# Performance work log

Measured on AMD Instinct MI355X. Metric: run time of the kernel, lower is better.

Reference implementation:

```python
import jax, jax.numpy as jnp
import numpy as np

H = 20  # GRU hidden size (fixed in the module)


def gru_cell(x, h, Wih, Whh, bih, bhh):
    # PyTorch GRU cell math. x: (B, F), h: (B, H)
    gi = x @ Wih.T + bih  # (B, 3H)
    gh = h @ Whh.T + bhh  # (B, 3H)
    i_r, i_z, i_n = jnp.split(gi, 3, axis=-1)
    h_r, h_z, h_n = jnp.split(gh, 3, axis=-1)
    r = jax.nn.sigmoid(i_r + h_r)
    z = jax.nn.sigmoid(i_z + h_z)
    n = jnp.tanh(i_n + r * h_n)
    return (1.0 - z) * n + z * h


def setup_inputs() -> dict:
    key = jax.random.key(0)
    ks = jax.random.split(key, 16)
    B, S, R = 1024, 1024, 12
    F = R + 4 + 4 + 8 + 8  # 36 = input_record_width + embedding output_dim
    x = jax.random.normal(ks[0], (B, S, R), dtype=jnp.float32)
    onehots = jax.random.randint(ks[1], (B, S, 4), 0, 10, dtype=jnp.int64)
    s = 0.1
    inp = {
        'x': x, 'onehots': onehots,
        'emb0': jax.random.normal(ks[2], (10, 4), jnp.float32) * s,
        'emb1': jax.random.normal(ks[3], (20, 4), jnp.float32) * s,
        'emb2': jax.random.normal(ks[4], (50, 8), jnp.float32) * s,
        'emb3': jax.random.normal(ks[5], (100, 8), jnp.float32) * s,
        'Wih1': jax.random.normal(ks[6], (3 * H, F), jnp.float32) * s,
        'Whh1': jax.random.normal(ks[7], (3 * H, H), jnp.float32) * s,
        'bih1': jax.random.normal(ks[8], (3 * H,), jnp.float32) * s,
        'bhh1': jax.random.normal(ks[9], (3 * H,), jnp.float32) * s,
        'Wih2': jax.random.normal(ks[10], (3 * H, F), jnp.float32) * s,
        'Whh2': jax.random.normal(ks[11], (3 * H, H), jnp.float32) * s,
        'bih2': jax.random.normal(ks[12], (3 * H,), jnp.float32) * s,
        'bhh2': jax.random.normal(ks[13], (3 * H,), jnp.float32) * s,
        'Wfc': jax.random.normal(ks[14], (F, H), jnp.float32) * s,
        'bfc': jax.random.normal(ks[15], (F,), jnp.float32) * s,
    }
    return inp


def reference(x, onehots, emb0, emb1, emb2, emb3,
              Wih1, Whh1, bih1, bhh1, Wih2, Whh2, bih2, bhh2, Wfc, bfc):
    # Onehot embedding: lookup per categorical column, concat
    emb = jnp.concatenate([
        emb0[onehots[..., 0]], emb1[onehots[..., 1]],
        emb2[onehots[..., 2]], emb3[onehots[..., 3]],
    ], axis=-1)
    xin = jnp.concatenate([x, emb], axis=-1)  # (B, S, F)
    origin = xin
    B, S, F = xin.shape

    # Encoder GRU (gru1) over the sequence; keep only final hidden state
    h0 = jnp.zeros((B, H), xin.dtype)

    def enc_step(h, xt):
        return gru_cell(xt, h, Wih1, Whh1, bih1, bhh1), None

    h_last, _ = jax.lax.scan(enc_step, h0, jnp.swapaxes(xin, 0, 1))
    h = jnp.tanh(h_last)
    x0 = jnp.tanh(h @ Wfc.T + bfc)  # first decoded step

    def dec_step(carry, _):
        xprev, hprev = carry
        hnew = jnp.tanh(gru_cell(xprev, hprev, Wih2, Whh2, bih2, bhh2))
        xnew = jnp.tanh(hnew @ Wfc.T + bfc)
        return (xnew, hnew), xnew

    _, rest = jax.lax.scan(dec_step, (x0, h), None, length=S - 1)  # (S-1, B, F)
    xs = jnp.concatenate([x0[None], rest], axis=0)  # (S, B, F)
    xs = jnp.swapaxes(xs, 0, 1)[:, ::-1]  # (B, S, F), flipped along time
    return (origin, xs)
```

## Files before the change

### kernel.cpp

```cpp
#include <hip/hip_runtime.h>

#define BATCH 1024
#define SEQ   1024
#define FDIM  36
#define HID   20
#define G3    60
#define CR    64
#define NCHUNK (SEQ/CR)

typedef float v2f __attribute__((ext_vector_type(2)));

__device__ __forceinline__ float fast_sigmoid(float x){
    return __builtin_amdgcn_rcpf(1.0f + __expf(-x));
}
__device__ __forceinline__ float fast_tanh(float x){
    return fmaf(-2.0f, __builtin_amdgcn_rcpf(1.0f + __expf(2.0f*x)), 1.0f);
}

__global__ __launch_bounds__(128, 2)
void gru_fused(const float* __restrict__ x,
               const int* __restrict__ oh,
               const float* __restrict__ e0, const float* __restrict__ e1,
               const float* __restrict__ e2, const float* __restrict__ e3,
               const float* __restrict__ Wih1g, const float* __restrict__ Whh1g,
               const float* __restrict__ bih1g, const float* __restrict__ bhh1g,
               const float* __restrict__ Wih2g, const float* __restrict__ Whh2g,
               const float* __restrict__ bih2g, const float* __restrict__ bhh2g,
               const float* __restrict__ Wfcg,  const float* __restrict__ bfcg,
               float* __restrict__ origin, float* __restrict__ out2)
{
    __shared__ __align__(16) float gbuf[2][CR][G3];
    __shared__ __align__(16) float psh[64];
    __shared__ __align__(16) float dsh[64];
    __shared__ __align__(16) float hsh[64];

    const int lane   = threadIdx.x & 63;
    const bool is_enc = (threadIdx.x < 64);
    const int b = __builtin_amdgcn_readfirstlane(blockIdx.x);

    const int k = lane < G3 ? lane : G3 - 1;

    float whh1[HID];
    float bh1 = 0.f;
    float hs[HID];
    float hv = 0.0f;
    if (is_enc) {
        #pragma unroll
        for (int u = 0; u < HID; u++) whh1[u] = Whh1g[k * HID + u];
        bh1 = bhh1g[k];
        #pragma unroll
        for (int u = 0; u < HID; u++) hs[u] = 0.0f;
    }

    const int j = lane;
    const float* tbl; int ohc, eshift, sub;
    if (j < 16)      { tbl = e0; ohc = 0; eshift = 2; sub = j - 12; }
    else if (j < 20) { tbl = e1; ohc = 1; eshift = 2; sub = j - 16; }
    else if (j < 28) { tbl = e2; ohc = 2; eshift = 3; sub = j - 20; }
    else             { tbl = e3; ohc = 3; eshift = 3; sub = j - 28; }
    if (sub < 0) sub = 0;
    if (sub > 7) sub = 7;
    const bool from_x = (j < 12);
    const float* pa = from_x ? (x + j) : (tbl + sub);
    v2f w1p[FDIM/2]; float bi1 = 0.f;
    if (!is_enc) {
        #pragma unroll
        for (int q = 0; q < FDIM/2; q++) w1p[q] = ((const v2f*)(Wih1g + k * FDIM))[q];
        bi1 = bih1g[k];
    }

#define HS_BCAST(HVAL) do {                                                  \
        hsh[lane] = (HVAL);                                                  \
        const float4* hq_ = (const float4*)hsh;                              \
        float4 t0_ = hq_[0], t1_ = hq_[1], t2_ = hq_[2], t3_ = hq_[3],       \
               t4_ = hq_[4];                                                 \
        hs[0]=t0_.x;  hs[1]=t0_.y;  hs[2]=t0_.z;  hs[3]=t0_.w;               \
        hs[4]=t1_.x;  hs[5]=t1_.y;  hs[6]=t1_.z;  hs[7]=t1_.w;               \
        hs[8]=t2_.x;  hs[9]=t2_.y;  hs[10]=t2_.z; hs[11]=t2_.w;              \
        hs[12]=t3_.x; hs[13]=t3_.y; hs[14]=t3_.z; hs[15]=t3_.w;              \
        hs[16]=t4_.x; hs[17]=t4_.y; hs[18]=t4_.z; hs[19]=t4_.w;              \
    } while (0)

#define GATE_STEP(GIV, WHH, BH, HVAR) do {                                   \
        float h0 = BH, h1 = 0.f, h2 = 0.f, h3 = 0.f;                         \
        _Pragma("unroll")                                                    \
        for (int uu = 0; uu < HID; uu += 4) {                                \
            h0 = fmaf(WHH[uu + 0], hs[uu + 0], h0);                          \
            h1 = fmaf(WHH[uu + 1], hs[uu + 1], h1);                          \
            h2 = fmaf(WHH[uu + 2], hs[uu + 2], h2);                          \
            h3 = fmaf(WHH[uu + 3], hs[uu + 3], h3);                          \
        }                                                                    \
        float gh = (h0 + h1) + (h2 + h3);                                    \
        float v   = (GIV) + gh;                                              \
        float in_ = __shfl((GIV),(lane + 40) & 63);                          \
        float hn  = __shfl(gh,   (lane + 40) & 63);                          \
        float s = fast_sigmoid(v);                        \
        float z = __shfl(s, (lane + 20) & 63);  \
        float n = fast_tanh(fmaf(s, hn, in_));                               \
        HVAR = n + z * (HVAR - n);                                           \
        HS_BCAST(HVAR);                                                      \
    } while (0)

#define CONSUME_CHUNK(CB) do {                                               \
        const float* gp = &gbuf[CB][0][k];                                   \
        float ga = gp[0], gbv = gp[G3];                                      \
        _Pragma("unroll 1")                                                  \
        for (int i = 0; i < CR; i += 2) {                                    \
            float ge = ga, go = gbv;                                         \
            if (i < CR - 2) ga = gp[(i + 2) * G3];                           \
            GATE_STEP(ge, whh1, bh1, hv);                                    \
            if (i < CR - 2) gbv = gp[(i + 3) * G3];                          \
            GATE_STEP(go, whh1, bh1, hv);                                    \
        }                                                                    \
    } while (0)

    #pragma unroll 1
    for (int c = 0; c < NCHUNK; ++c) {
        if (!is_enc) {
            const int rbase = b * SEQ + c * CR;
            float* gdst = &gbuf[c & 1][0][0];
            const float4* xp4 = (const float4*)psh;
            #pragma unroll 1
            for (int g = 0; g < CR / 8; ++g) {
                int ohv[8];
                #pragma unroll
                for (int n = 0; n < 8; n++)
                    ohv[n] = oh[(rbase + 8 * g + n) * 4 + ohc];
                float valv[8];
                #pragma unroll
                for (int n = 0; n < 8; n++) {
                    int R = rbase + 8 * g + n;
                    int off = from_x ? (R * 12) : (ohv[n] << eshift);
                    valv[n] = pa[off];
                }
                #pragma unroll
                for (int n = 0; n < 8; n++) {
                    const int i = 8 * g + n;
                    const size_t R = (size_t)(rbase + i);
                    psh[lane] = valv[n];
                    if (lane < FDIM) origin[R * FDIM + lane] = valv[n];
                    v2f a0 = {bi1, 0.f}, a1 = {0.f, 0.f};
                    #pragma unroll
                    for (int q = 0; q < 9; q++) {
                        float4 xv4 = xp4[q];
                        v2f xlo = {xv4.x, xv4.y}, xhi = {xv4.z, xv4.w};
                        a0 = __builtin_elementwise_fma(w1p[2*q],     xlo, a0);
                        a1 = __builtin_elementwise_fma(w1p[2*q + 1], xhi, a1);
                    }
                    float gg = (a0.x + a1.x) + (a0.y + a1.y);
                    if (lane < G3) gdst[i * G3 + lane] = gg;
                }
            }
        } else if (c > 0) {
            CONSUME_CHUNK((c - 1) & 1);
        }
        __syncthreads();
    }
    if (!is_enc) return;

    CONSUME_CHUNK((NCHUNK - 1) & 1);

    const int kf = lane < FDIM ? lane : FDIM - 1;
    float whh2[HID], wfc[HID];
    v2f wih2p[FDIM/2];
    #pragma unroll
    for (int q = 0; q < FDIM/2; q++) wih2p[q] = ((const v2f*)(Wih2g + k * FDIM))[q];
    #pragma unroll
    for (int u = 0; u < HID; u++) whh2[u] = Whh2g[k * HID + u];
    #pragma unroll
    for (int u = 0; u < HID; u++) wfc[u] = Wfcg[kf * HID + u];
    const float bi2 = bih2g[k], bh2 = bhh2g[k];
    const float bf  = bfcg[kf];

    float hvd = fast_tanh(hv);
    HS_BCAST(hvd);

    float* orow = out2 + ((size_t)b * SEQ + (SEQ - 1)) * FDIM;
    const v2f* xp = (const v2f*)dsh;

    float xv0;
    {
        float f0 = bf, f1 = 0.f, f2 = 0.f, f3 = 0.f;
        #pragma unroll
        for (int u = 0; u < HID; u += 4) {
            f0 = fmaf(wfc[u + 0], hs[u + 0], f0);
            f1 = fmaf(wfc[u + 1], hs[u + 1], f1);
            f2 = fmaf(wfc[u + 2], hs[u + 2], f2);
            f3 = fmaf(wfc[u + 3], hs[u + 3], f3);
        }
        xv0 = fast_tanh((f0 + f1) + (f2 + f3));
    }
    dsh[lane] = xv0;
    v2f xsA[FDIM/2], xsB[FDIM/2];
    #pragma unroll
    for (int q = 0; q < FDIM/2; q++) xsA[q] = xp[q];
    if (lane < FDIM) orow[lane] = xv0;

#define DEC_STEP(XSIN, XSOUT, XST) do {                                      \
        float h0 = bh2, h1 = 0.f, h2 = 0.f, h3 = 0.f;                        \
        _Pragma("unroll")                                                    \
        for (int u = 0; u < HID; u += 4) {                                   \
            h0 = fmaf(whh2[u + 0], hs[u + 0], h0);                           \
            h1 = fmaf(whh2[u + 1], hs[u + 1], h1);                           \
            h2 = fmaf(whh2[u + 2], hs[u + 2], h2);                           \
            h3 = fmaf(whh2[u + 3], hs[u + 3], h3);                           \
        }                                                                    \
        float gh = (h0 + h1) + (h2 + h3);                                    \
        v2f accA = {bi2, 0.f}, accB = {0.f, 0.f};                            \
        _Pragma("unroll")                                                    \
        for (int q = 0; q < FDIM/2; q += 2) {                                \
            accA = __builtin_elementwise_fma(wih2p[q],     XSIN[q],     accA); \
            accB = __builtin_elementwise_fma(wih2p[q + 1], XSIN[q + 1], accB); \
        }                                                                    \
        float gi = (accA.x + accB.x) + (accA.y + accB.y);                    \
        float v   = gi + gh;                                                 \
        float in_ = __shfl(gi, (lane + 40) & 63);                            \
        float hn  = __shfl(gh, (lane + 40) & 63);                            \
        float s = fast_sigmoid(v);                                           \
        float z = __shfl(s, (lane + 20) & 63);                               \
        float n = fast_tanh(fmaf(s, hn, in_));                               \
        float hraw = n + z * (hvd - n);                                      \
        hvd = fast_tanh(hraw);                                               \
        HS_BCAST(hvd);                                                       \
        float f0 = bf, f1 = 0.f, f2 = 0.f, f3 = 0.f;                         \
        _Pragma("unroll")                                                    \
        for (int u = 0; u < HID; u += 4) {                                   \
            f0 = fmaf(wfc[u + 0], hs[u + 0], f0);                            \
            f1 = fmaf(wfc[u + 1], hs[u + 1], f1);                            \
            f2 = fmaf(wfc[u + 2], hs[u + 2], f2);                            \
            f3 = fmaf(wfc[u + 3], hs[u + 3], f3);                            \
        }                                                                    \
        XST = fast_tanh((f0 + f1) + (f2 + f3));                              \
        orow -= FDIM;                                                        \
        dsh[lane] = XST;                  \
        _Pragma("unroll")                                                    \
        for (int q = 0; q < FDIM/2; q++) XSOUT[q] = xp[q];    \
        if (lane < FDIM) orow[lane] = XST;                                   \
    } while (0)

    float xvA, xvB;
    #pragma unroll 1
    for (int i = 0; i < (SEQ - 2) / 2; ++i) {
        DEC_STEP(xsA, xsB, xvA);
        DEC_STEP(xsB, xsA, xvB);
    }
    DEC_STEP(xsA, xsB, xvA);
}

extern "C" void kernel_launch(void* const* d_in, const int* in_sizes, int n_in,
                              void* d_out, int out_size, void* d_ws, size_t ws_size,
                              hipStream_t stream) {
    const float* x    = (const float*)d_in[0];
    const int*   oh   = (const int*)d_in[1];
    const float* e0   = (const float*)d_in[2];
    const float* e1   = (const float*)d_in[3];
    const float* e2   = (const float*)d_in[4];
    const float* e3   = (const float*)d_in[5];
    const float* Wih1 = (const float*)d_in[6];
    const float* Whh1 = (const float*)d_in[7];
    const float* bih1 = (const float*)d_in[8];
    const float* bhh1 = (const float*)d_in[9];
    const float* Wih2 = (const float*)d_in[10];
    const float* Whh2 = (const float*)d_in[11];
    const float* bih2 = (const float*)d_in[12];
    const float* bhh2 = (const float*)d_in[13];
    const float* Wfc  = (const float*)d_in[14];
    const float* bfc  = (const float*)d_in[15];

    float* out    = (float*)d_out;
    float* origin = out;
    float* out2   = out + (size_t)BATCH * SEQ * FDIM;

    gru_fused<<<BATCH, 128, 0, stream>>>(x, oh, e0, e1, e2, e3,
                                         Wih1, Whh1, bih1, bhh1,
                                         Wih2, Whh2, bih2, bhh2,
                                         Wfc, bfc, origin, out2);
}
```

Before: 993.4 us.

## Process two batch rows per block to interleave independent recurrences

Measured after the change: 1.488 ms. 49.7% more time.

```diff
diff --git a/kernel.cpp b/kernel.cpp
--- a/kernel.cpp
+++ b/kernel.cpp
@@ -17,7 +17,7 @@
     return fmaf(-2.0f, __builtin_amdgcn_rcpf(1.0f + __expf(2.0f*x)), 1.0f);
 }
 
-__global__ __launch_bounds__(128, 2)
+__global__ __launch_bounds__(128, 1)
 void gru_fused(const float* __restrict__ x,
                const int* __restrict__ oh,
                const float* __restrict__ e0, const float* __restrict__ e1,
@@ -29,27 +29,28 @@
                const float* __restrict__ Wfcg,  const float* __restrict__ bfcg,
                float* __restrict__ origin, float* __restrict__ out2)
 {
-    __shared__ __align__(16) float gbuf[2][CR][G3];
-    __shared__ __align__(16) float psh[64];
-    __shared__ __align__(16) float dsh[64];
-    __shared__ __align__(16) float hsh[64];
+    __shared__ __align__(16) float gbuf[2][2][CR][G3];
+    __shared__ __align__(16) float psh[2][64];
+    __shared__ __align__(16) float dsh[2][64];
+    __shared__ __align__(16) float hsh[2][64];
 
     const int lane   = threadIdx.x & 63;
     const bool is_enc = (threadIdx.x < 64);
-    const int b = __builtin_amdgcn_readfirstlane(blockIdx.x);
+    const int bb = __builtin_amdgcn_readfirstlane(blockIdx.x);
+    const int b0 = 2 * bb, b1 = 2 * bb + 1;
 
     const int k = lane < G3 ? lane : G3 - 1;
 
     float whh1[HID];
     float bh1 = 0.f;
-    float hs[HID];
-    float hv = 0.0f;
+    float hsA[HID], hsB[HID];
+    float hvA = 0.0f, hvB = 0.0f;
     if (is_enc) {
         #pragma unroll
         for (int u = 0; u < HID; u++) whh1[u] = Whh1g[k * HID + u];
         bh1 = bhh1g[k];
         #pragma unroll
-        for (int u = 0; u < HID; u++) hs[u] = 0.0f;
+        for (int u = 0; u < HID; u++) { hsA[u] = 0.0f; hsB[u] = 0.0f; }
     }
 
     const int j = lane;
@@ -69,86 +70,93 @@
         bi1 = bih1g[k];
     }
 
-#define HS_BCAST(HVAL) do {                                                  \
-        hsh[lane] = (HVAL);                                                  \
-        const float4* hq_ = (const float4*)hsh;                              \
+#define HS_BCAST(P, HVAL, HS) do {                                           \
+        hsh[P][lane] = (HVAL);                                               \
+        const float4* hq_ = (const float4*)hsh[P];                           \
         float4 t0_ = hq_[0], t1_ = hq_[1], t2_ = hq_[2], t3_ = hq_[3],       \
                t4_ = hq_[4];                                                 \
-        hs[0]=t0_.x;  hs[1]=t0_.y;  hs[2]=t0_.z;  hs[3]=t0_.w;               \
-        hs[4]=t1_.x;  hs[5]=t1_.y;  hs[6]=t1_.z;  hs[7]=t1_.w;               \
-        hs[8]=t2_.x;  hs[9]=t2_.y;  hs[10]=t2_.z; hs[11]=t2_.w;              \
-        hs[12]=t3_.x; hs[13]=t3_.y; hs[14]=t3_.z; hs[15]=t3_.w;              \
-        hs[16]=t4_.x; hs[17]=t4_.y; hs[18]=t4_.z; hs[19]=t4_.w;              \
-    } while (0)
-
-#define GATE_STEP(GIV, WHH, BH, HVAR) do {                                   \
-        float h0 = BH, h1 = 0.f, h2 = 0.f, h3 = 0.f;                         \
+        HS[0]=t0_.x;  HS[1]=t0_.y;  HS[2]=t0_.z;  HS[3]=t0_.w;               \
+        HS[4]=t1_.x;  HS[5]=t1_.y;  HS[6]=t1_.z;  HS[7]=t1_.w;               \
+        HS[8]=t2_.x;  HS[9]=t2_.y;  HS[10]=t2_.z; HS[11]=t2_.w;              \
+        HS[12]=t3_.x; HS[13]=t3_.y; HS[14]=t3_.z; HS[15]=t3_.w;              \
+        HS[16]=t4_.x; HS[17]=t4_.y; HS[18]=t4_.z; HS[19]=t4_.w;              \
+    } while (0)
+
+#define GATE_STEP(GIV, HS, HVAR, P) do {                                     \
+        float h0 = bh1, h1 = 0.f, h2 = 0.f, h3 = 0.f;                        \
         _Pragma("unroll")                                                    \
         for (int uu = 0; uu < HID; uu += 4) {                                \
-            h0 = fmaf(WHH[uu + 0], hs[uu + 0], h0);                          \
-            h1 = fmaf(WHH[uu + 1], hs[uu + 1], h1);                          \
-            h2 = fmaf(WHH[uu + 2], hs[uu + 2], h2);                          \
-            h3 = fmaf(WHH[uu + 3], hs[uu + 3], h3);                          \
+            h0 = fmaf(whh1[uu + 0], HS[uu + 0], h0);                         \
+            h1 = fmaf(whh1[uu + 1], HS[uu + 1], h1);                         \
+            h2 = fmaf(whh1[uu + 2], HS[uu + 2], h2);                         \
+            h3 = fmaf(whh1[uu + 3], HS[uu + 3], h3);                         \
         }                                                                    \
         float gh = (h0 + h1) + (h2 + h3);                                    \
         float v   = (GIV) + gh;                                              \
         float in_ = __shfl((GIV),(lane + 40) & 63);                          \
         float hn  = __shfl(gh,   (lane + 40) & 63);                          \
-        float s = fast_sigmoid(v);                        \
-        float z = __shfl(s, (lane + 20) & 63);  \
+        float s = fast_sigmoid(v);                                           \
+        float z = __shfl(s, (lane + 20) & 63);                               \
         float n = fast_tanh(fmaf(s, hn, in_));                               \
         HVAR = n + z * (HVAR - n);                                           \
-        HS_BCAST(HVAR);                                                      \
+        HS_BCAST(P, HVAR, HS);                                               \
     } while (0)
 
 #define CONSUME_CHUNK(CB) do {                                               \
-        const float* gp = &gbuf[CB][0][k];                                   \
-        float ga = gp[0], gbv = gp[G3];                                      \
+        const float* gpA = &gbuf[0][CB][0][k];                               \
+        const float* gpB = &gbuf[1][CB][0][k];                               \
+        float gA0 = gpA[0],  gB0 = gpB[0];                                   \
+        float gA1 = gpA[G3], gB1 = gpB[G3];                                  \
         _Pragma("unroll 1")                                                  \
         for (int i = 0; i < CR; i += 2) {                                    \
-            float ge = ga, go = gbv;                                         \
-            if (i < CR - 2) ga = gp[(i + 2) * G3];                           \
-            GATE_STEP(ge, whh1, bh1, hv);                                    \
-            if (i < CR - 2) gbv = gp[(i + 3) * G3];                          \
-            GATE_STEP(go, whh1, bh1, hv);                                    \
+            float eA = gA0, eB = gB0, oA = gA1, oB = gB1;                    \
+            if (i < CR - 2) { gA0 = gpA[(i + 2) * G3]; gB0 = gpB[(i + 2) * G3]; } \
+            GATE_STEP(eA, hsA, hvA, 0);                                      \
+            GATE_STEP(eB, hsB, hvB, 1);                                      \
+            if (i < CR - 2) { gA1 = gpA[(i + 3) * G3]; gB1 = gpB[(i + 3) * G3]; } \
+            GATE_STEP(oA, hsA, hvA, 0);                                      \
+            GATE_STEP(oB, hsB, hvB, 1);                                      \
         }                                                                    \
     } while (0)
 
     #pragma unroll 1
     for (int c = 0; c < NCHUNK; ++c) {
         if (!is_enc) {
-            const int rbase = b * SEQ + c * CR;
-            float* gdst = &gbuf[c & 1][0][0];
-            const float4* xp4 = (const float4*)psh;
             #pragma unroll 1
-            for (int g = 0; g < CR / 8; ++g) {
-                int ohv[8];
-                #pragma unroll
-                for (int n = 0; n < 8; n++)
-                    ohv[n] = oh[(rbase + 8 * g + n) * 4 + ohc];
-                float valv[8];
-                #pragma unroll
-                for (int n = 0; n < 8; n++) {
-                    int R = rbase + 8 * g + n;
-                    int off = from_x ? (R * 12) : (ohv[n] << eshift);
-                    valv[n] = pa[off];
-                }
-                #pragma unroll
-                for (int n = 0; n < 8; n++) {
-                    const int i = 8 * g + n;
-                    const size_t R = (size_t)(rbase + i);
-                    psh[lane] = valv[n];
-                    if (lane < FDIM) origin[R * FDIM + lane] = valv[n];
-                    v2f a0 = {bi1, 0.f}, a1 = {0.f, 0.f};
+            for (int p = 0; p < 2; ++p) {
+                const int rbase = (p ? b1 : b0) * SEQ + c * CR;
+                float* gdst = &gbuf[p][c & 1][0][0];
+                const float4* xp4 = (const float4*)psh[p];
+                #pragma unroll 1
+                for (int g = 0; g < CR / 8; ++g) {
+                    int ohv[8];
                     #pragma unroll
-                    for (int q = 0; q < 9; q++) {
-                        float4 xv4 = xp4[q];
-                        v2f xlo = {xv4.x, xv4.y}, xhi = {xv4.z, xv4.w};
-                        a0 = __builtin_elementwise_fma(w1p[2*q],     xlo, a0);
-                        a1 = __builtin_elementwise_fma(w1p[2*q + 1], xhi, a1);
+                    for (int n = 0; n < 8; n++)
+                        ohv[n] = oh[(rbase + 8 * g + n) * 4 + ohc];
+                    float valv[8];
+                    #pragma unroll
+                    for (int n = 0; n < 8; n++) {
+                        int R = rbase + 8 * g + n;
+                        int off = from_x ? (R * 12) : (ohv[n] << eshift);
+                        valv[n] = pa[off];
                     }
-                    float gg = (a0.x + a1.x) + (a0.y + a1.y);
-                    if (lane < G3) gdst[i * G3 + lane] = gg;
+                    #pragma unroll
+                    for (int n = 0; n < 8; n++) {
+                        const int i = 8 * g + n;
+                        const size_t R = (size_t)(rbase + i);
+                        psh[p][lane] = valv[n];
+                        if (lane < FDIM) origin[R * FDIM + lane] = valv[n];
+                        v2f a0 = {bi1, 0.f}, a1 = {0.f, 0.f};
+                        #pragma unroll
+                        for (int q = 0; q < 9; q++) {
+                            float4 xv4 = xp4[q];
+                            v2f xlo = {xv4.x, xv4.y}, xhi = {xv4.z, xv4.w};
+                            a0 = __builtin_elementwise_fma(w1p[2*q],     xlo, a0);
+                            a1 = __builtin_elementwise_fma(w1p[2*q + 1], xhi, a1);
+                        }
+                        float gg = (a0.x + a1.x) + (a0.y + a1.y);
+                        if (lane < G3) gdst[i * G3 + lane] = gg;
+                    }
                 }
             }
         } else if (c > 0) {
@@ -172,45 +180,53 @@
     const float bi2 = bih2g[k], bh2 = bhh2g[k];
     const float bf  = bfcg[kf];
 
-    float hvd = fast_tanh(hv);
-    HS_BCAST(hvd);
-
-    float* orow = out2 + ((size_t)b * SEQ + (SEQ - 1)) * FDIM;
-    const v2f* xp = (const v2f*)dsh;
-
-    float xv0;
-    {
-        float f0 = bf, f1 = 0.f, f2 = 0.f, f3 = 0.f;
-        #pragma unroll
-        for (int u = 0; u < HID; u += 4) {
-            f0 = fmaf(wfc[u + 0], hs[u + 0], f0);
-            f1 = fmaf(wfc[u + 1], hs[u + 1], f1);
-            f2 = fmaf(wfc[u + 2], hs[u + 2], f2);
-            f3 = fmaf(wfc[u + 3], hs[u + 3], f3);
-        }
-        xv0 = fast_tanh((f0 + f1) + (f2 + f3));
-    }
-    dsh[lane] = xv0;
-    v2f xsA[FDIM/2], xsB[FDIM/2];
-    #pragma unroll
-    for (int q = 0; q < FDIM/2; q++) xsA[q] = xp[q];
-    if (lane < FDIM) orow[lane] = xv0;
-
-#define DEC_STEP(XSIN, XSOUT, XST) do {                                      \
+    float hvdA = fast_tanh(hvA);
+    float hvdB = fast_tanh(hvB);
+    HS_BCAST(0, hvdA, hsA);
+    HS_BCAST(1, hvdB, hsB);
+
+    float* orowA = out2 + ((size_t)b0 * SEQ + (SEQ - 1)) * FDIM + kf;
+    float* orowB = out2 + ((size_t)b1 * SEQ + (SEQ - 1)) * FDIM + kf;
+
+#define FC_STEP(HS, XOUT) do {                                               \
+        float f0 = bf, f1 = 0.f, f2 = 0.f, f3 = 0.f;                         \
+        _Pragma("unroll")                                                    \
+        for (int u = 0; u < HID; u += 4) {                                   \
+            f0 = fmaf(wfc[u + 0], HS[u + 0], f0);                            \
+            f1 = fmaf(wfc[u + 1], HS[u + 1], f1);                            \
+            f2 = fmaf(wfc[u + 2], HS[u + 2], f2);                            \
+            f3 = fmaf(wfc[u + 3], HS[u + 3], f3);                            \
+        }                                                                    \
+        XOUT = fast_tanh((f0 + f1) + (f2 + f3));                             \
+    } while (0)
+
+    float xvA, xvB;
+    FC_STEP(hsA, xvA);
+    FC_STEP(hsB, xvB);
+    dsh[0][lane] = xvA;
+    dsh[1][lane] = xvB;
+    *orowA = xvA;
+    *orowB = xvB;
+
+#define DEC_STEP(P, HS, HVD, OROW) do {                                      \
+        const v2f* xp_ = (const v2f*)dsh[P];                                 \
+        v2f xs2[FDIM/2];                                                     \
+        _Pragma("unroll")                                                    \
+        for (int q = 0; q < FDIM/2; q++) xs2[q] = xp_[q];                    \
         float h0 = bh2, h1 = 0.f, h2 = 0.f, h3 = 0.f;                        \
         _Pragma("unroll")                                                    \
         for (int u = 0; u < HID; u += 4) {                                   \
-            h0 = fmaf(whh2[u + 0], hs[u + 0], h0);                           \
-            h1 = fmaf(whh2[u + 1], hs[u + 1], h1);                           \
-            h2 = fmaf(whh2[u + 2], hs[u + 2], h2);                           \
-            h3 = fmaf(whh2[u + 3], hs[u + 3], h3);                           \
+            h0 = fmaf(whh2[u + 0], HS[u + 0], h0);                           \
+            h1 = fmaf(whh2[u + 1], HS[u + 1], h1);                           \
+            h2 = fmaf(whh2[u + 2], HS[u + 2], h2);                           \
+            h3 = fmaf(whh2[u + 3], HS[u + 3], h3);                           \
         }                                                                    \
         float gh = (h0 + h1) + (h2 + h3);                                    \
         v2f accA = {bi2, 0.f}, accB = {0.f, 0.f};                            \
         _Pragma("unroll")                                                    \
         for (int q = 0; q < FDIM/2; q += 2) {                                \
-            accA = __builtin_elementwise_fma(wih2p[q],     XSIN[q],     accA); \
-            accB = __builtin_elementwise_fma(wih2p[q + 1], XSIN[q + 1], accB); \
+            accA = __builtin_elementwise_fma(wih2p[q],     xs2[q],     accA); \
+            accB = __builtin_elementwise_fma(wih2p[q + 1], xs2[q + 1], accB); \
         }                                                                    \
         float gi = (accA.x + accB.x) + (accA.y + accB.y);                    \
         float v   = gi + gh;                                                 \
@@ -219,32 +235,21 @@
         float s = fast_sigmoid(v);                                           \
         float z = __shfl(s, (lane + 20) & 63);                               \
         float n = fast_tanh(fmaf(s, hn, in_));                               \
-        float hraw = n + z * (hvd - n);                                      \
-        hvd = fast_tanh(hraw);                                               \
-        HS_BCAST(hvd);                                                       \
-        float f0 = bf, f1 = 0.f, f2 = 0.f, f3 = 0.f;                         \
-        _Pragma("unroll")                                                    \
-        for (int u = 0; u < HID; u += 4) {                                   \
-            f0 = fmaf(wfc[u + 0], hs[u + 0], f0);                            \
-            f1 = fmaf(wfc[u + 1], hs[u + 1], f1);                            \
-            f2 = fmaf(wfc[u + 2], hs[u + 2], f2);                            \
-            f3 = fmaf(wfc[u + 3], hs[u + 3], f3);                            \
-        }                                                                    \
-        XST = fast_tanh((f0 + f1) + (f2 + f3));                              \
-        orow -= FDIM;                                                        \
-        dsh[lane] = XST;                  \
-        _Pragma("unroll")                                                    \
-        for (int q = 0; q < FDIM/2; q++) XSOUT[q] = xp[q];    \
-        if (lane < FDIM) orow[lane] = XST;                                   \
-    } while (0)
-
-    float xvA, xvB;
+        float hraw = n + z * (HVD - n);                                      \
+        HVD = fast_tanh(hraw);                                               \
+        HS_BCAST(P, HVD, HS);                                                \
+        float xnew;                                                          \
+        FC_STEP(HS, xnew);                                                   \
+        OROW -= FDIM;                                                        \
+        dsh[P][lane] = xnew;                                                 \
+        *OROW = xnew;                                                        \
+    } while (0)
+
     #pragma unroll 1
-    for (int i = 0; i < (SEQ - 2) / 2; ++i) {
-        DEC_STEP(xsA, xsB, xvA);
-        DEC_STEP(xsB, xsA, xvB);
-    }
-    DEC_STEP(xsA, xsB, xvA);
+    for (int d = 1; d < SEQ; ++d) {
+        DEC_STEP(0, hsA, hvdA, orowA);
+        DEC_STEP(1, hsB, hvdB, orowB);
+    }
 }
 
 extern "C" void kernel_launch(void* const* d_in, const int* in_sizes, int n_in,
@@ -271,8 +276,8 @@
     float* origin = out;
     float* out2   = out + (size_t)BATCH * SEQ * FDIM;
 
-    gru_fused<<<BATCH, 128, 0, stream>>>(x, oh, e0, e1, e2, e3,
-                                         Wih1, Whh1, bih1, bhh1,
-                                         Wih2, Whh2, bih2, bhh2,
-                                         Wfc, bfc, origin, out2);
-}
+    gru_fused<<<BATCH/2, 128, 0, stream>>>(x, oh, e0, e1, e2, e3,
+                                           Wih1, Whh1, bih1, bhh1,
+                                           Wih2, Whh2, bih2, bhh2,
+                                           Wfc, bfc, origin, out2);
+}
```
